# Optimization experiments

Measured on AMD Instinct MI355X. Metric: run time of the kernel, lower is better.

The kernel has to match this reference:

```python
import jax, jax.numpy as jnp
import numpy as np

B, V, J, NB = 512, 6890, 24, 10
P = (J - 1) * 9  # 207 pose-blendshape features
# Standard SMPL kinematic tree (parents[0] = -1 for root)
PARENTS = np.array([-1, 0, 0, 0, 1, 2, 3, 4, 5, 6, 7, 8, 9, 9, 9, 12, 13, 14, 16, 17, 18, 19, 20, 21])


def rodrigues(aa):
    """Axis-angle [N,3] -> rotation matrices [N,3,3] (batch_rodrigues)."""
    angle = jnp.linalg.norm(aa, axis=-1, keepdims=True) + 1e-8
    axis = aa / angle
    x, y, z = axis[..., 0], axis[..., 1], axis[..., 2]
    zero = jnp.zeros_like(x)
    K = jnp.stack([zero, -z, y, z, zero, -x, -y, x, zero], axis=-1).reshape(aa.shape[0], 3, 3)
    s = jnp.sin(angle)[..., None]
    c = jnp.cos(angle)[..., None]
    return jnp.eye(3, dtype=aa.dtype) + s * K + (1.0 - c) * jnp.matmul(K, K)


def setup_inputs() -> dict:
    key = jax.random.key(0)
    ks = jax.random.split(key, 9)
    J_reg = jax.random.uniform(ks[7], (J, V), dtype=jnp.float32)
    J_reg = J_reg / jnp.sum(J_reg, axis=1, keepdims=True)
    W = jax.nn.softmax(4.0 * jax.random.normal(ks[8], (V, J), dtype=jnp.float32), axis=-1)
    return {
        "betas": jax.random.normal(ks[0], (B, NB), dtype=jnp.float32),
        "body_pose": 0.3 * jax.random.normal(ks[1], (B, (J - 1) * 3), dtype=jnp.float32),
        "global_orient": 0.3 * jax.random.normal(ks[2], (B, 3), dtype=jnp.float32),
        "transl": jax.random.normal(ks[3], (B, 3), dtype=jnp.float32),
        "v_template": jax.random.normal(ks[4], (V, 3), dtype=jnp.float32),
        "shapedirs": 0.01 * jax.random.normal(ks[5], (V, 3, NB), dtype=jnp.float32),
        "posedirs": 0.01 * jax.random.normal(ks[6], (P, V * 3), dtype=jnp.float32),
        "J_regressor": J_reg,
        "lbs_weights": W,
    }


def reference(betas, body_pose, global_orient, transl, v_template, shapedirs, posedirs, J_regressor, lbs_weights):
    b = betas.shape[0]
    # --- pose to rotation matrices (pose2rot=True path) ---
    full_pose = jnp.concatenate([global_orient, body_pose], axis=-1)  # [B, 72]
    rot_mats = rodrigues(full_pose.reshape(-1, 3)).reshape(b, J, 3, 3)
    # --- shape blend shapes ---
    v_shaped = v_template + jnp.einsum('bl,vcl->bvc', betas, shapedirs)  # [B,V,3]
    joints = jnp.einsum('jv,bvc->bjc', J_regressor, v_shaped)            # [B,J,3]
    # --- pose blend shapes ---
    pose_feature = (rot_mats[:, 1:] - jnp.eye(3, dtype=rot_mats.dtype)).reshape(b, P)
    v_posed = v_shaped + (pose_feature @ posedirs).reshape(b, V, 3)
    # --- kinematic chain (batch_rigid_transform) ---
    rel_joints = joints.at[:, 1:].add(-joints[:, PARENTS[1:]])
    top = jnp.concatenate([rot_mats, rel_joints[..., None]], axis=-1)   # [B,J,3,4]
    bottom = jnp.broadcast_to(jnp.array([0.0, 0.0, 0.0, 1.0], dtype=rot_mats.dtype), (b, J, 1, 4))
    mats = jnp.concatenate([top, bottom], axis=-2)                      # [B,J,4,4]
    chain = [mats[:, 0]]
    for i in range(1, J):  # fixed 24-joint serial composition
        chain.append(chain[PARENTS[i]] @ mats[:, i])
    A = jnp.stack(chain, axis=1)                                        # [B,J,4,4]
    posed_joints = A[..., :3, 3]
    # remove rest-pose joint locations from the transforms
    t_rel = A[..., :3, 3] - jnp.einsum('bjmn,bjn->bjm', A[..., :3, :3], joints)
    A_rel = A.at[..., :3, 3].set(t_rel)
    # --- linear blend skinning ---
    T = jnp.einsum('vj,bjmn->bvmn', lbs_weights, A_rel)                 # [B,V,4,4]
    verts = jnp.einsum('bvmn,bvn->bvm', T[..., :3, :3], v_posed) + T[..., :3, 3]
    vertices = verts + transl[:, None]
    joints_out = posed_joints + transl[:, None]
    return vertices, joints_out
```

## Files before the change

### kernel.cpp

```cpp
#include <hip/hip_runtime.h>
#include <hip/hip_bf16.h>
#include <math.h>

#define Bn 512
#define Vn 6890
#define NBn 10
#define Pn 207
#define N3n 20670
#define KP 224
#define VPAD 6912

typedef __attribute__((ext_vector_type(8))) _Float16 half8;
typedef __attribute__((ext_vector_type(4))) float f32x4;

__constant__ int c_par[24] = {-1,0,0,0,1,2,3,4,5,6,7,8,9,9,9,12,13,14,16,17,18,19,20,21};
__constant__ int c_lvl[10] = {0,1,4,7,10,15,18,20,22,24};


__global__ __launch_bounds__(256) void k_prep(
    const float* __restrict__ Jreg, const float* __restrict__ vtpl,
    const float* __restrict__ sdirs, const float* __restrict__ pdirs,
    const float* __restrict__ W, float* __restrict__ part,
    _Float16* __restrict__ B_h, _Float16* __restrict__ W_h)
{
  const int tid = threadIdx.x;
  if (blockIdx.x < 192) {
    const int j = blockIdx.x % 24;
    const int chunk = blockIdx.x / 24;
    const int lane = tid & 63, wv = tid >> 6;
    const int vlo = chunk * 862;
    const int vhi = min(Vn, vlo + 862);
    __shared__ float wred[4][33];
    float acc[33];
#pragma unroll
    for (int k = 0; k < 33; k++) acc[k] = 0.f;
    for (int v = vlo + tid; v < vhi; v += 256) {
      float w = Jreg[(size_t)j * Vn + v];
      const float* sp = sdirs + (size_t)v * 30;
#pragma unroll
      for (int c = 0; c < 3; c++) {
#pragma unroll
        for (int l = 0; l < 10; l++) acc[c*11 + l] += w * sp[c*10 + l];
        acc[c*11 + 10] += w * vtpl[v*3 + c];
      }
    }
#pragma unroll
    for (int k = 0; k < 33; k++) {
      float s = acc[k];
      for (int off = 32; off > 0; off >>= 1) s += __shfl_xor(s, off);
      if (lane == 0) wred[wv][k] = s;
    }
    __syncthreads();
    if (tid < 33) {
      float s = wred[0][tid] + wred[1][tid] + wred[2][tid] + wred[3][tid];
      int c = tid / 11, k = tid % 11;
      part[(size_t)chunk * 792 + (j*3 + c) * 11 + k] = s;
    }
  } else if (blockIdx.x < 192 + 2268) {
    const int pair = (blockIdx.x - 192) * 4 + (tid >> 6);
    const int l = tid & 63;
    const int nt = pair / 7, s = pair % 7;
    const int col = nt * 16 + (l & 15);
    const int kb = s * 32 + ((l >> 4) << 3);
    half8 hv;
#pragma unroll
    for (int j = 0; j < 8; j++) {
      int k = kb + j;
      float f = 0.f;
      if (col < N3n) {
        if (k < Pn) f = pdirs[(size_t)k * N3n + col];
        else if (k < 217) f = sdirs[(size_t)col * 10 + (k - 207)];
        else if (k == 217) f = (float)(_Float16)vtpl[col];
        else if (k == 218) {
          float t = vtpl[col];
          f = t - (float)(_Float16)t;
        }
      }
      hv[j] = (_Float16)f;
    }
    *(half8*)(B_h + (size_t)pair * 512 + l * 8) = hv;
  } else {
    int idx = (blockIdx.x - 192 - 2268) * 256 + tid;
    if (idx < VPAD * 32) {
      int v = idx >> 5, k = idx & 31;
      float f;
      if (v < Vn && k < 24) f = W[(size_t)v * 24 + k];
      else if (k == 24)     f = 1.0f;
      else                  f = 0.f;
      W_h[idx] = (_Float16)f;
    }
  }
}

__global__ __launch_bounds__(512) void k_pose2(
    const float* __restrict__ betas, const float* __restrict__ body_pose,
    const float* __restrict__ gorient, const float* __restrict__ transl,
    const float* __restrict__ part,
    _Float16* __restrict__ pf_h, _Float16* __restrict__ Ar_h,
    float* __restrict__ out_joints)
{
  const int tid = threadIdx.x;
  const int wave = tid >> 6;
  const int lane = tid & 63;
  const int b = blockIdx.x * 8 + wave;

  __shared__ float JS_s[720];
  __shared__ float Jt_s[72];
  __shared__ float Rs[8][24][9];
  __shared__ float jnt[8][24][3];
  __shared__ float rel[8][24][3];
  __shared__ float A_s[8][24][12];

  for (int idx = tid; idx < 792; idx += 512) {
    float s = 0.f;
#pragma unroll
    for (int y = 0; y < 8; y++) s += part[(size_t)y * 792 + idx];
    int bid = idx / 11, k = idx % 11;
    if (k < 10) JS_s[bid * 10 + k] = s;
    else        Jt_s[bid] = s;
  }

  if (lane < 24) {
    float x, y, z;
    if (lane == 0) { x = gorient[b*3+0]; y = gorient[b*3+1]; z = gorient[b*3+2]; }
    else { int o = b*69 + (lane-1)*3; x = body_pose[o]; y = body_pose[o+1]; z = body_pose[o+2]; }
    float ang = sqrtf(x*x + y*y + z*z) + 1e-8f;
    float inv = 1.0f / ang;
    float ux = x*inv, uy = y*inv, uz = z*inv;
    float s = sinf(ang), cc = cosf(ang), omc = 1.0f - cc;
    float K[9] = {0.f, -uz, uy,  uz, 0.f, -ux,  -uy, ux, 0.f};
#pragma unroll
    for (int mm = 0; mm < 3; mm++)
#pragma unroll
      for (int nn = 0; nn < 3; nn++) {
        float kk = K[mm*3+0]*K[0+nn] + K[mm*3+1]*K[3+nn] + K[mm*3+2]*K[6+nn];
        float eye = (mm == nn) ? 1.0f : 0.0f;
        Rs[wave][lane][mm*3+nn] = eye + s*K[mm*3+nn] + omc*kk;
      }
  }
  __syncthreads();

  for (int idx = lane; idx < 72; idx += 64) {
    float a = Jt_s[idx];
#pragma unroll
    for (int l = 0; l < 10; l++) a += betas[b*10 + l] * JS_s[idx*10 + l];
    jnt[wave][idx/3][idx%3] = a;
  }
  for (int idx = lane; idx < KP; idx += 64) {
    float f = 0.f;
    if (idx < Pn) {
      int j = 1 + idx / 9, e = idx % 9;
      float eye = (e == 0 || e == 4 || e == 8) ? 1.0f : 0.0f;
      f = Rs[wave][j][e] - eye;
    } else if (idx < 217) {
      f = betas[b*10 + (idx - 207)];
    } else if (idx < 219) {
      f = 1.0f;
    }
    pf_h[(size_t)b * KP + idx] = (_Float16)f;
  }
  __syncthreads();
  for (int idx = lane; idx < 72; idx += 64) {
    int j = idx/3, cc = idx%3;
    float r = jnt[wave][j][cc];
    if (j > 0) r -= jnt[wave][c_par[j]][cc];
    rel[wave][j][cc] = r;
  }
  __syncthreads();
  if (lane < 12) {
    int m = lane/4, nn = lane%4;
    A_s[wave][0][lane] = (nn < 3) ? Rs[wave][0][m*3+nn] : rel[wave][0][m];
  }
  __syncthreads();
  for (int lev = 1; lev <= 8; lev++) {
    const int s0 = c_lvl[lev], s1 = c_lvl[lev + 1];
    const int jj = lane / 12, r = lane % 12;
    if (jj < s1 - s0) {
      const int i = s0 + jj;
      const int p = c_par[i];
      const int m = r >> 2, nn = r & 3;
      float v;
      if (nn < 3)
        v = A_s[wave][p][m*4+0]*Rs[wave][i][0+nn] + A_s[wave][p][m*4+1]*Rs[wave][i][3+nn] + A_s[wave][p][m*4+2]*Rs[wave][i][6+nn];
      else
        v = A_s[wave][p][m*4+0]*rel[wave][i][0] + A_s[wave][p][m*4+1]*rel[wave][i][1] + A_s[wave][p][m*4+2]*rel[wave][i][2] + A_s[wave][p][m*4+3];
      A_s[wave][i][r] = v;
    }
    __syncthreads();
  }
  for (int idx = lane; idx < 72; idx += 64) {
    int j = idx/3, cc = idx%3;
    out_joints[(size_t)b * 72 + idx] = A_s[wave][j][cc*4+3] + transl[b*3+cc];
  }
  for (int idx = lane; idx < 512; idx += 64) {
    int e = idx >> 5, k = idx & 31;
    float a = 0.f;
    if (e < 12 && k < 24) {
      int m = e >> 2, nn = e & 3;
      if (nn < 3) a = A_s[wave][k][m*4+nn];
      else a = A_s[wave][k][m*4+3] - (A_s[wave][k][m*4+0]*jnt[wave][k][0] + A_s[wave][k][m*4+1]*jnt[wave][k][1] + A_s[wave][k][m*4+2]*jnt[wave][k][2]);
    } else if (k == 24 && e < 12 && (e & 3) == 3) {
      a = transl[b*3 + (e >> 2)];
    }
    Ar_h[(size_t)b * 512 + idx] = (_Float16)a;
  }
}

__global__ __launch_bounds__(256) void k_mm4(
    const _Float16* __restrict__ pf_h, const _Float16* __restrict__ B_h,
    const _Float16* __restrict__ W_h, const _Float16* __restrict__ Ar_h,
    float* __restrict__ out)
{
  const int lin = blockIdx.x;
  const int r8 = lin & 7;
  const int k2 = lin >> 3;
  const int b_t = k2 & 15;
  const int m8 = k2 >> 4;
  const int v_t = r8 * 14 + m8;
  if (v_t >= 108) return;

  const int tid = threadIdx.x;
  const int l = tid & 63;
  const int wave = tid >> 6;
  const int b0 = b_t * 32;
  const int v0 = v_t * 64;

  __shared__ __align__(16) _Float16 vp[32][196];

  const int c0 = l & 15;
  const int kk0 = (l >> 4) << 3;
  const int ntb = v_t * 12 + wave * 3;
  f32x4 acc[2][3];
#pragma unroll
  for (int t = 0; t < 2; t++)
#pragma unroll
    for (int n = 0; n < 3; n++) acc[t][n] = (f32x4){0.f, 0.f, 0.f, 0.f};

#pragma unroll
  for (int s = 0; s < 7; s++) {
    half8 bv[3];
#pragma unroll
    for (int n = 0; n < 3; n++)
      bv[n] = *(const half8*)(B_h + ((size_t)(ntb + n) * 7 + s) * 512 + l * 8);
#pragma unroll
    for (int t = 0; t < 2; t++) {
      half8 fa = *(const half8*)(pf_h + (size_t)(b0 + t * 16 + c0) * KP + kk0 + s * 32);
#pragma unroll
      for (int n = 0; n < 3; n++)
        acc[t][n] = __builtin_amdgcn_mfma_f32_16x16x32_f16(fa, bv[n], acc[t][n], 0, 0, 0);
    }
  }
  {
    const int colb = wave * 48 + c0;
    const int rowb = (l >> 4) * 4;
#pragma unroll
    for (int t = 0; t < 2; t++)
#pragma unroll
      for (int n = 0; n < 3; n++)
#pragma unroll
        for (int r = 0; r < 4; r++)
          vp[t * 16 + rowb + r][colb + n * 16] = (_Float16)acc[t][n][r];
  }
  __syncthreads();

  const int c = l & 15;
  const int g = l >> 4;
  const int kk = g << 3;

  half8 wh[4];
#pragma unroll
  for (int mt = 0; mt < 4; mt++)
    wh[mt] = *(const half8*)(W_h + (size_t)(v0 + mt * 16 + c) * 32 + kk);

#pragma unroll
  for (int i = 0; i < 8; i++) {
    const int bl = wave * 8 + i;
    half8 ah = *(const half8*)(Ar_h + (size_t)(b0 + bl) * 512 + c * 32 + kk);
#pragma unroll
    for (int mt = 0; mt < 4; mt++) {
      f32x4 t = {0.f, 0.f, 0.f, 0.f};
      t = __builtin_amdgcn_mfma_f32_16x16x32_f16(ah, wh[mt], t, 0, 0, 0);
      const int vl2 = mt * 16 + c;
      const int v = v0 + vl2;
      if (g < 3 && v < Vn) {
        float x = (float)vp[bl][3 * vl2 + 0];
        float y = (float)vp[bl][3 * vl2 + 1];
        float z = (float)vp[bl][3 * vl2 + 2];
        out[((size_t)(b0 + bl) * Vn + v) * 3 + g] = t[0]*x + t[1]*y + t[2]*z + t[3];
      }
    }
  }
}


__global__ __launch_bounds__(256) void k_jsjt_part(
    const float* __restrict__ Jreg, const float* __restrict__ vtpl,
    const float* __restrict__ sdirs, float* __restrict__ part)
{
  const int bid = blockIdx.x;
  const int chunk = blockIdx.y;
  const int j = bid / 3, c = bid % 3;
  const int tid = threadIdx.x;
  const int vlo = chunk * 862;
  const int vhi = min(Vn, vlo + 862);
  float acc[11];
#pragma unroll
  for (int k = 0; k < 11; k++) acc[k] = 0.f;
  for (int v = vlo + tid; v < vhi; v += 256) {
    float w = Jreg[(size_t)j * Vn + v];
    int n = v * 3 + c;
#pragma unroll
    for (int l = 0; l < 10; l++) acc[l] += w * sdirs[(size_t)n * 10 + l];
    acc[10] += w * vtpl[n];
  }
  __shared__ float red[256];
  for (int k = 0; k < 11; k++) {
    red[tid] = acc[k];
    __syncthreads();
    for (int s = 128; s > 0; s >>= 1) {
      if (tid < s) red[tid] += red[tid + s];
      __syncthreads();
    }
    if (tid == 0) part[(size_t)chunk * 792 + bid * 11 + k] = red[0];
    __syncthreads();
  }
}

__global__ __launch_bounds__(1024) void k_jsjt_red(
    const float* __restrict__ part, float* __restrict__ JS, float* __restrict__ Jt)
{
  const int t = threadIdx.x;
  if (t >= 792) return;
  float s = 0.f;
#pragma unroll
  for (int y = 0; y < 8; y++) s += part[(size_t)y * 792 + t];
  int bid = t / 11, k = t % 11;
  if (k < 10) JS[bid * 10 + k] = s;
  else        Jt[bid] = s;
}

__global__ __launch_bounds__(64) void k_pose_fb(
    const float* __restrict__ betas, const float* __restrict__ body_pose,
    const float* __restrict__ gorient, const float* __restrict__ transl,
    const float* __restrict__ JS, const float* __restrict__ Jt,
    float* __restrict__ pf_ws, float* __restrict__ Ar_ws,
    float* __restrict__ out_joints)
{
  const int b = blockIdx.x;
  const int tid = threadIdx.x;
  __shared__ float Rs[24][9];
  __shared__ float jnt[24][3];
  __shared__ float rel[24][3];
  __shared__ float A_s[24][12];

  if (tid < 24) {
    float x, y, z;
    if (tid == 0) { x = gorient[b*3+0]; y = gorient[b*3+1]; z = gorient[b*3+2]; }
    else { int o = b*69 + (tid-1)*3; x = body_pose[o]; y = body_pose[o+1]; z = body_pose[o+2]; }
    float ang = sqrtf(x*x + y*y + z*z) + 1e-8f;
    float inv = 1.0f / ang;
    float ux = x*inv, uy = y*inv, uz = z*inv;
    float s = sinf(ang), cc = cosf(ang), omc = 1.0f - cc;
    float K[9] = {0.f, -uz, uy,  uz, 0.f, -ux,  -uy, ux, 0.f};
#pragma unroll
    for (int mm = 0; mm < 3; mm++)
#pragma unroll
      for (int nn = 0; nn < 3; nn++) {
        float kk = K[mm*3+0]*K[0+nn] + K[mm*3+1]*K[3+nn] + K[mm*3+2]*K[6+nn];
        float eye = (mm == nn) ? 1.0f : 0.0f;
        Rs[tid][mm*3+nn] = eye + s*K[mm*3+nn] + omc*kk;
      }
  }
  for (int idx = tid; idx < 72; idx += 64) {
    float a = Jt[idx];
#pragma unroll
    for (int l = 0; l < 10; l++) a += betas[b*10 + l] * JS[idx*10 + l];
    jnt[idx/3][idx%3] = a;
  }
  __syncthreads();
  for (int idx = tid; idx < Pn; idx += 64) {
    int j = 1 + idx / 9, e = idx % 9;
    float eye = (e == 0 || e == 4 || e == 8) ? 1.0f : 0.0f;
    pf_ws[(size_t)b * Pn + idx] = Rs[j][e] - eye;
  }
  for (int idx = tid; idx < 72; idx += 64) {
    int j = idx/3, cc = idx%3;
    float r = jnt[j][cc];
    if (j > 0) r -= jnt[c_par[j]][cc];
    rel[j][cc] = r;
  }
  __syncthreads();
  if (tid < 12) {
    int m = tid/4, nn = tid%4;
    A_s[0][tid] = (nn < 3) ? Rs[0][m*3+nn] : rel[0][m];
  }
  __syncthreads();
  for (int i = 1; i < 24; i++) {
    if (tid < 12) {
      int m = tid/4, nn = tid%4;
      int p = c_par[i];
      float v;
      if (nn < 3)
        v = A_s[p][m*4+0]*Rs[i][0+nn] + A_s[p][m*4+1]*Rs[i][3+nn] + A_s[p][m*4+2]*Rs[i][6+nn];
      else
        v = A_s[p][m*4+0]*rel[i][0] + A_s[p][m*4+1]*rel[i][1] + A_s[p][m*4+2]*rel[i][2] + A_s[p][m*4+3];
      A_s[i][tid] = v;
    }
    __syncthreads();
  }
  for (int idx = tid; idx < 72; idx += 64) {
    int j = idx/3, cc = idx%3;
    out_joints[(size_t)b * 72 + idx] = A_s[j][cc*4+3] + transl[b*3+cc];
  }
  for (int idx = tid; idx < 288; idx += 64) {
    int j = idx/12, r = idx%12, m = r/4, nn = r%4;
    float v;
    if (nn < 3) v = A_s[j][m*4+nn];
    else v = A_s[j][m*4+3] - (A_s[j][m*4+0]*jnt[j][0] + A_s[j][m*4+1]*jnt[j][1] + A_s[j][m*4+2]*jnt[j][2]);
    Ar_ws[(size_t)b * 288 + idx] = v;
  }
}

__global__ __launch_bounds__(192) void k_verts_fb(
    const float* __restrict__ betas, const float* __restrict__ transl,
    const float* __restrict__ vtpl, const float* __restrict__ sdirs,
    const float* __restrict__ pdirs, const float* __restrict__ W,
    const float* __restrict__ pf_ws, const float* __restrict__ Ar_ws,
    float* __restrict__ out)
{
  const int tid = threadIdx.x;
  const int b0 = blockIdx.x * 16;
  const int v0 = blockIdx.y * 128;
  const int n0 = v0 * 3;
  __shared__ __align__(16) float pf_s[Pn][16];
  __shared__ __align__(16) float Ar_s[16][288];
  __shared__ __align__(16) float vp_s[16][384];
  __shared__ float betas_s[16][NBn];
  __shared__ float transl_s[16][3];
  for (int idx = tid; idx < Pn * 16; idx += 192) {
    int p = idx >> 4, bi = idx & 15;
    pf_s[p][bi] = pf_ws[(size_t)(b0 + bi) * Pn + p];
  }
  for (int idx = tid; idx < 16 * 288; idx += 192)
    Ar_s[idx / 288][idx % 288] = Ar_ws[(size_t)b0 * 288 + idx];
  for (int idx = tid; idx < 16 * NBn; idx += 192)
    betas_s[idx / NBn][idx % NBn] = betas[(size_t)b0 * NBn + idx];
  for (int idx = tid; idx < 48; idx += 192)
    transl_s[idx / 3][idx % 3] = transl[(size_t)b0 * 3 + idx];
  __syncthreads();
  const int n = n0 + 2 * tid;
  const bool valid = (n < N3n);
  float acc0[16], acc1[16];
#pragma unroll
  for (int i = 0; i < 16; i++) { acc0[i] = 0.f; acc1[i] = 0.f; }
  for (int p = 0; p < Pn; p++) {
    float pd0 = 0.f, pd1 = 0.f;
    if (valid) { float2 t = *(const float2*)(pdirs + (size_t)p * N3n + n); pd0 = t.x; pd1 = t.y; }
    const float4* row = (const float4*)(pf_s[p]);
#pragma unroll
    for (int q = 0; q < 4; q++) {
      float4 f = row[q];
      acc0[4*q+0] += f.x * pd0;  acc1[4*q+0] += f.x * pd1;
      acc0[4*q+1] += f.y * pd0;  acc1[4*q+1] += f.y * pd1;
      acc0[4*q+2] += f.z * pd0;  acc1[4*q+2] += f.z * pd1;
      acc0[4*q+3] += f.w * pd0;  acc1[4*q+3] += f.w * pd1;
    }
  }
  float sd0[10], sd1[10], vt0 = 0.f, vt1 = 0.f;
#pragma unroll
  for (int l = 0; l < 10; l++) { sd0[l] = 0.f; sd1[l] = 0.f; }
  if (valid) {
    for (int l = 0; l < 10; l++) { sd0[l] = sdirs[(size_t)n*10 + l]; sd1[l] = sdirs[(size_t)n*10 + 10 + l]; }
    vt0 = vtpl[n]; vt1 = vtpl[n+1];
  }
#pragma unroll
  for (int bi = 0; bi < 16; bi++) {
    float s0 = vt0, s1 = vt1;
#pragma unroll
    for (int l = 0; l < 10; l++) { float bb = betas_s[bi][l]; s0 += bb*sd0[l]; s1 += bb*sd1[l]; }
    acc0[bi] += s0; acc1[bi] += s1;
  }
#pragma unroll
  for (int bi = 0; bi < 16; bi++) { vp_s[bi][2*tid] = acc0[bi]; vp_s[bi][2*tid+1] = acc1[bi]; }
  __syncthreads();
  const int m = tid / 64;
  const int vl = tid % 64;
  const int va = v0 + vl, vb = v0 + vl + 64;
  const bool va_ok = (va < Vn), vb_ok = (vb < Vn);
  float Wr0[24], Wr1[24];
#pragma unroll
  for (int j = 0; j < 24; j++) { Wr0[j] = 0.f; Wr1[j] = 0.f; }
  if (va_ok) { const float4* wp = (const float4*)(W + (size_t)va*24);
#pragma unroll
    for (int q = 0; q < 6; q++) { float4 f = wp[q]; Wr0[4*q]=f.x; Wr0[4*q+1]=f.y; Wr0[4*q+2]=f.z; Wr0[4*q+3]=f.w; } }
  if (vb_ok) { const float4* wp = (const float4*)(W + (size_t)vb*24);
#pragma unroll
    for (int q = 0; q < 6; q++) { float4 f = wp[q]; Wr1[4*q]=f.x; Wr1[4*q+1]=f.y; Wr1[4*q+2]=f.z; Wr1[4*q+3]=f.w; } }
  for (int bi = 0; bi < 16; bi++) {
    float Ta0=0.f,Ta1=0.f,Ta2=0.f,Ta3=0.f, Tb0=0.f,Tb1=0.f,Tb2=0.f,Tb3=0.f;
    const float4* arb = (const float4*)(Ar_s[bi]);
#pragma unroll
    for (int j = 0; j < 24; j++) {
      float4 a = arb[j*3 + m];
      float wa = Wr0[j], wb = Wr1[j];
      Ta0 += wa*a.x; Ta1 += wa*a.y; Ta2 += wa*a.z; Ta3 += wa*a.w;
      Tb0 += wb*a.x; Tb1 += wb*a.y; Tb2 += wb*a.z; Tb3 += wb*a.w;
    }
    float tr = transl_s[bi][m];
    if (va_ok) {
      float x = vp_s[bi][vl*3+0], y = vp_s[bi][vl*3+1], z = vp_s[bi][vl*3+2];
      out[((size_t)(b0+bi)*Vn + va)*3 + m] = Ta0*x + Ta1*y + Ta2*z + Ta3 + tr;
    }
    if (vb_ok) {
      float x = vp_s[bi][(vl+64)*3+0], y = vp_s[bi][(vl+64)*3+1], z = vp_s[bi][(vl+64)*3+2];
      out[((size_t)(b0+bi)*Vn + vb)*3 + m] = Tb0*x + Tb1*y + Tb2*z + Tb3 + tr;
    }
  }
}

extern "C" void kernel_launch(void* const* d_in, const int* in_sizes, int n_in,
                              void* d_out, int out_size, void* d_ws, size_t ws_size,
                              hipStream_t stream)
{
  const float *betas=nullptr, *bpose=nullptr, *gorient=nullptr, *transl=nullptr,
              *vtpl=nullptr, *sdirs=nullptr, *pdirs=nullptr, *Jreg=nullptr, *W=nullptr;
  int seen1536 = 0, seen165360 = 0;
  for (int i = 0; i < n_in; i++) {
    const float* p = (const float*)d_in[i];
    switch (in_sizes[i]) {
      case 5120:    betas = p; break;
      case 35328:   bpose = p; break;
      case 20670:   vtpl  = p; break;
      case 206700:  sdirs = p; break;
      case 4278690: pdirs = p; break;
      case 1536:    if (seen1536++ == 0) gorient = p; else transl = p; break;
      case 165360:  if (seen165360++ == 0) Jreg = p; else W = p; break;
      default: break;
    }
  }
  float* out = (float*)d_out;

  float* ws   = (float*)d_ws;
  float* part = ws;
  float* JS   = ws + 6336;
  float* Jt   = ws + 7056;
  float* pf   = ws + 7128;
  float* Ar   = ws + 113112;
  _Float16* pf_h = (_Float16*)(ws + 260568);
  _Float16* B_h  = (_Float16*)(ws + 317912);
  _Float16* W_h  = (_Float16*)(ws + 2640344);
  _Float16* Ar_h = (_Float16*)(ws + 2861528);
  const size_t WS_NEED = (size_t)3123672 * 4;
  const bool big = (ws_size >= WS_NEED);

  if (big) {
    k_prep<<<3324, 256, 0, stream>>>(Jreg, vtpl, sdirs, pdirs, W, part, B_h, W_h);
    k_pose2<<<64, 512, 0, stream>>>(betas, bpose, gorient, transl, part,
                                    pf_h, Ar_h, out + (size_t)Bn * Vn * 3);
    k_mm4<<<1792, 256, 0, stream>>>(pf_h, B_h, W_h, Ar_h, out);
  } else {
    k_jsjt_part<<<dim3(72, 8), 256, 0, stream>>>(Jreg, vtpl, sdirs, part);
    k_jsjt_red<<<1, 1024, 0, stream>>>(part, JS, Jt);
    k_pose_fb<<<Bn, 64, 0, stream>>>(betas, bpose, gorient, transl, JS, Jt, pf, Ar,
                                     out + (size_t)Bn * Vn * 3);
    k_verts_fb<<<dim3(32, 54), 192, 0, stream>>>(betas, transl, vtpl, sdirs,
                                                 pdirs, W, pf, Ar, out);
  }
}
```

Before: 58.64 us.

## Stage posedirs through shared tiles, keep fp32 swizzled vp, shrink pose blocks

```diff
diff --git a/kernel.cpp b/kernel.cpp
--- a/kernel.cpp
+++ b/kernel.cpp
@@ -24,13 +24,15 @@
     _Float16* __restrict__ B_h, _Float16* __restrict__ W_h)
 {
   const int tid = threadIdx.x;
+  __shared__ float wred[4][33];
+  __shared__ __align__(16) float tile[224][36];
+
   if (blockIdx.x < 192) {
     const int j = blockIdx.x % 24;
     const int chunk = blockIdx.x / 24;
     const int lane = tid & 63, wv = tid >> 6;
     const int vlo = chunk * 862;
     const int vhi = min(Vn, vlo + 862);
-    __shared__ float wred[4][33];
     float acc[33];
 #pragma unroll
     for (int k = 0; k < 33; k++) acc[k] = 0.f;
@@ -56,31 +58,49 @@
       int c = tid / 11, k = tid % 11;
       part[(size_t)chunk * 792 + (j*3 + c) * 11 + k] = s;
     }
-  } else if (blockIdx.x < 192 + 2268) {
-    const int pair = (blockIdx.x - 192) * 4 + (tid >> 6);
-    const int l = tid & 63;
-    const int nt = pair / 7, s = pair % 7;
-    const int col = nt * 16 + (l & 15);
-    const int kb = s * 32 + ((l >> 4) << 3);
-    half8 hv;
-#pragma unroll
-    for (int j = 0; j < 8; j++) {
-      int k = kb + j;
+  } else if (blockIdx.x < 840) {
+    const int p = blockIdx.x - 192;
+    const int cols0 = p * 32;
+    for (int idx = tid; idx < 207 * 8; idx += 256) {
+      int row = idx >> 3, cq = (idx & 7) << 2;
+      int gc = cols0 + cq;
+      float4 v4 = {0.f, 0.f, 0.f, 0.f};
+      if (gc + 3 < N3n) {
+        v4 = *(const float4*)(pdirs + (size_t)row * N3n + gc);
+      } else if (gc < N3n) {
+        float t[4];
+#pragma unroll
+        for (int e = 0; e < 4; e++) t[e] = (gc + e < N3n) ? pdirs[(size_t)row * N3n + gc + e] : 0.f;
+        v4 = make_float4(t[0], t[1], t[2], t[3]);
+      }
+      *(float4*)&tile[row][cq] = v4;
+    }
+    for (int idx = tid; idx < 17 * 32; idx += 256) {
+      int r = idx >> 5, cc = idx & 31;
+      int k = 207 + r;
+      int gc = cols0 + cc;
       float f = 0.f;
-      if (col < N3n) {
-        if (k < Pn) f = pdirs[(size_t)k * N3n + col];
-        else if (k < 217) f = sdirs[(size_t)col * 10 + (k - 207)];
-        else if (k == 217) f = (float)(_Float16)vtpl[col];
-        else if (k == 218) {
-          float t = vtpl[col];
-          f = t - (float)(_Float16)t;
-        }
-      }
-      hv[j] = (_Float16)f;
-    }
-    *(half8*)(B_h + (size_t)pair * 512 + l * 8) = hv;
+      if (gc < N3n) {
+        if (k < 217)      f = sdirs[(size_t)gc * 10 + (k - 207)];
+        else if (k == 217) f = (float)(_Float16)vtpl[gc];
+        else if (k == 218) { float tv = vtpl[gc]; f = tv - (float)(_Float16)tv; }
+      }
+      tile[k][cc] = f;
+    }
+    __syncthreads();
+    for (int idx = tid; idx < 896; idx += 256) {
+      int pl = idx >> 6;
+      int l  = idx & 63;
+      int ntl = pl / 7, s = pl % 7;
+      int colc = ntl * 16 + (l & 15);
+      int kb = s * 32 + ((l >> 4) << 3);
+      half8 hv;
+#pragma unroll
+      for (int j = 0; j < 8; j++) hv[j] = (_Float16)tile[kb + j][colc];
+      *(half8*)(B_h + ((size_t)(2 * p + ntl) * 7 + s) * 512 + (size_t)l * 8) = hv;
+    }
   } else {
-    int idx = (blockIdx.x - 192 - 2268) * 256 + tid;
+    int idx = (blockIdx.x - 840) * 256 + tid;
     if (idx < VPAD * 32) {
       int v = idx >> 5, k = idx & 31;
       float f;
@@ -92,7 +112,7 @@
   }
 }
 
-__global__ __launch_bounds__(512) void k_pose2(
+__global__ __launch_bounds__(256) void k_pose2(
     const float* __restrict__ betas, const float* __restrict__ body_pose,
     const float* __restrict__ gorient, const float* __restrict__ transl,
     const float* __restrict__ part,
@@ -102,16 +122,16 @@
   const int tid = threadIdx.x;
   const int wave = tid >> 6;
   const int lane = tid & 63;
-  const int b = blockIdx.x * 8 + wave;
+  const int b = blockIdx.x * 4 + wave;
 
   __shared__ float JS_s[720];
   __shared__ float Jt_s[72];
-  __shared__ float Rs[8][24][9];
-  __shared__ float jnt[8][24][3];
-  __shared__ float rel[8][24][3];
-  __shared__ float A_s[8][24][12];
-
-  for (int idx = tid; idx < 792; idx += 512) {
+  __shared__ float Rs[4][24][9];
+  __shared__ float jnt[4][24][3];
+  __shared__ float rel[4][24][3];
+  __shared__ float A_s[4][24][12];
+
+  for (int idx = tid; idx < 792; idx += 256) {
     float s = 0.f;
 #pragma unroll
     for (int y = 0; y < 8; y++) s += part[(size_t)y * 792 + idx];
@@ -206,7 +226,7 @@
   }
 }
 
-__global__ __launch_bounds__(256) void k_mm4(
+__global__ __launch_bounds__(256) void k_mm5(
     const _Float16* __restrict__ pf_h, const _Float16* __restrict__ B_h,
     const _Float16* __restrict__ W_h, const _Float16* __restrict__ Ar_h,
     float* __restrict__ out)
@@ -225,7 +245,7 @@
   const int b0 = b_t * 32;
   const int v0 = v_t * 64;
 
-  __shared__ __align__(16) _Float16 vp[32][196];
+  __shared__ __align__(16) float vpT[192 * 32];
 
   const int c0 = l & 15;
   const int kk0 = (l >> 4) << 3;
@@ -251,42 +271,50 @@
     }
   }
   {
-    const int colb = wave * 48 + c0;
-    const int rowb = (l >> 4) * 4;
+    const int rowq = (l >> 4) * 4;
 #pragma unroll
     for (int t = 0; t < 2; t++)
 #pragma unroll
-      for (int n = 0; n < 3; n++)
-#pragma unroll
-        for (int r = 0; r < 4; r++)
-          vp[t * 16 + rowb + r][colb + n * 16] = (_Float16)acc[t][n][r];
-  }
-  __syncthreads();
-
-  const int c = l & 15;
+      for (int n = 0; n < 3; n++) {
+        const int col = wave * 48 + n * 16 + c0;
+        const int rowb = t * 16 + rowq;
+        *(f32x4*)&vpT[col * 32 + (rowb ^ ((col & 7) << 2))] = acc[t][n];
+      }
+  }
+  __syncthreads();
+
+  const int c = c0;
   const int g = l >> 4;
   const int kk = g << 3;
 
-  half8 wh[4];
+  half8 wh[4], ah[8];
 #pragma unroll
   for (int mt = 0; mt < 4; mt++)
     wh[mt] = *(const half8*)(W_h + (size_t)(v0 + mt * 16 + c) * 32 + kk);
-
-#pragma unroll
-  for (int i = 0; i < 8; i++) {
-    const int bl = wave * 8 + i;
-    half8 ah = *(const half8*)(Ar_h + (size_t)(b0 + bl) * 512 + c * 32 + kk);
-#pragma unroll
-    for (int mt = 0; mt < 4; mt++) {
-      f32x4 t = {0.f, 0.f, 0.f, 0.f};
-      t = __builtin_amdgcn_mfma_f32_16x16x32_f16(ah, wh[mt], t, 0, 0, 0);
-      const int vl2 = mt * 16 + c;
-      const int v = v0 + vl2;
-      if (g < 3 && v < Vn) {
-        float x = (float)vp[bl][3 * vl2 + 0];
-        float y = (float)vp[bl][3 * vl2 + 1];
-        float z = (float)vp[bl][3 * vl2 + 2];
-        out[((size_t)(b0 + bl) * Vn + v) * 3 + g] = t[0]*x + t[1]*y + t[2]*z + t[3];
+#pragma unroll
+  for (int i = 0; i < 8; i++)
+    ah[i] = *(const half8*)(Ar_h + (size_t)(b0 + wave * 8 + i) * 512 + c * 32 + kk);
+
+#pragma unroll
+  for (int mt = 0; mt < 4; mt++) {
+    const int vl2 = mt * 16 + c;
+    const int v = v0 + vl2;
+    const bool ok = (g < 3) && (v < Vn);
+    const int colx = 3 * vl2, coly = colx + 1, colz = colx + 2;
+#pragma unroll
+    for (int q = 0; q < 2; q++) {
+      const int rb = wave * 8 + q * 4;
+      f32x4 X = *(const f32x4*)&vpT[colx * 32 + (rb ^ ((colx & 7) << 2))];
+      f32x4 Y = *(const f32x4*)&vpT[coly * 32 + (rb ^ ((coly & 7) << 2))];
+      f32x4 Z = *(const f32x4*)&vpT[colz * 32 + (rb ^ ((colz & 7) << 2))];
+#pragma unroll
+      for (int r = 0; r < 4; r++) {
+        f32x4 t = {0.f, 0.f, 0.f, 0.f};
+        t = __builtin_amdgcn_mfma_f32_16x16x32_f16(ah[q * 4 + r], wh[mt], t, 0, 0, 0);
+        if (ok) {
+          const int bl = wave * 8 + q * 4 + r;
+          out[((size_t)(b0 + bl) * Vn + v) * 3 + g] = t[0]*X[r] + t[1]*Y[r] + t[2]*Z[r] + t[3];
+        }
       }
     }
   }
@@ -554,10 +582,10 @@
   const bool big = (ws_size >= WS_NEED);
 
   if (big) {
-    k_prep<<<3324, 256, 0, stream>>>(Jreg, vtpl, sdirs, pdirs, W, part, B_h, W_h);
-    k_pose2<<<64, 512, 0, stream>>>(betas, bpose, gorient, transl, part,
-                                    pf_h, Ar_h, out + (size_t)Bn * Vn * 3);
-    k_mm4<<<1792, 256, 0, stream>>>(pf_h, B_h, W_h, Ar_h, out);
+    k_prep<<<1704, 256, 0, stream>>>(Jreg, vtpl, sdirs, pdirs, W, part, B_h, W_h);
+    k_pose2<<<128, 256, 0, stream>>>(betas, bpose, gorient, transl, part,
+                                     pf_h, Ar_h, out + (size_t)Bn * Vn * 3);
+    k_mm5<<<1792, 256, 0, stream>>>(pf_h, B_h, W_h, Ar_h, out);
   } else {
     k_jsjt_part<<<dim3(72, 8), 256, 0, stream>>>(Jreg, vtpl, sdirs, part);
     k_jsjt_red<<<1, 1024, 0, stream>>>(part, JS, Jt);
```

New measurement: 53.32 us (median of 3 runs). 9.1% less time.
